# Performance work log

Measured on AMD Instinct MI355X. Metric: run time of the kernel, lower is better.

The kernel has to match this reference:

```python
import jax, jax.numpy as jnp
import numpy as np

E, D, H, O, K = 8, 1024, 4096, 1024, 2
N = 4096


def setup_inputs() -> dict:
    key = jax.random.key(0)
    ks = jax.random.split(key, 8)
    s_in = 1.0 / np.sqrt(D)
    s_h = 1.0 / np.sqrt(H)
    return {
        "x": jax.random.normal(ks[0], (N, D), dtype=jnp.float32),
        "W1": jax.random.uniform(ks[1], (E, D, H), jnp.float32, -s_in, s_in),
        "b1": jax.random.uniform(ks[2], (E, H), jnp.float32, -s_in, s_in),
        "W2": jax.random.uniform(ks[3], (E, H, O), jnp.float32, -s_h, s_h),
        "b2": jax.random.uniform(ks[4], (E, O), jnp.float32, -s_h, s_h),
        "Wg": jax.random.uniform(ks[5], (D, E), jnp.float32, -s_in, s_in),
        "bg": jax.random.uniform(ks[6], (E,), jnp.float32, -s_in, s_in),
    }


def reference(x, W1, b1, W2, b2, Wg, bg):
    # gate: [N, E] -> top-k logits and expert ids
    gate_logits = x @ Wg + bg
    topv, topi = jax.lax.top_k(gate_logits, K)          # [N, K]
    weights = jax.nn.softmax(topv, axis=-1)             # softmax over the k selected logits

    # dense all-expert MLP, then gather the selected experts per token
    h = jax.nn.relu(jnp.einsum("nd,edh->enh", x, W1) + b1[:, None, :])  # [E, N, H]
    y = jnp.einsum("enh,eho->eno", h, W2) + b2[:, None, :]              # [E, N, O]

    sel = y[topi, jnp.arange(N)[:, None]]               # [N, K, O]
    return jnp.sum(weights[..., None] * sel, axis=1)    # [N, O]
```

## Files before the change

kernel.cpp:

```cpp
#include <hip/hip_runtime.h>
#include <hip/hip_bf16.h>
#include <cstdint>

typedef __bf16 bf16;
typedef bf16 bf16x8 __attribute__((ext_vector_type(8)));
typedef bf16 bf16x4 __attribute__((ext_vector_type(4)));
typedef float f32x4 __attribute__((ext_vector_type(4)));

#define N_TOK 4096
#define DIM   1024
#define HID   4096
#define OUTD  1024
#define NEXP  8

__device__ __forceinline__ void async_copy16(const void* g, void* l) {
  __builtin_amdgcn_global_load_lds(
      (const __attribute__((address_space(1))) void*)g,
      (__attribute__((address_space(3))) void*)l, 16, 0, 0);
}

__device__ __forceinline__ void stage_tile2(
    const bf16* pA0, const bf16* pA1, const bf16* pA2, const bf16* pA3,
    const bf16* pB0, const bf16* pB1, const bf16* pB2, const bf16* pB3,
    bf16* lA, bf16* lB, int ko, int wave)
{
  async_copy16(pA0 + ko, lA + (wave * 4 + 0) * 512);
  async_copy16(pA1 + ko, lA + (wave * 4 + 1) * 512);
  async_copy16(pA2 + ko, lA + (wave * 4 + 2) * 512);
  async_copy16(pA3 + ko, lA + (wave * 4 + 3) * 512);
  async_copy16(pB0 + ko, lB + (wave * 4 + 0) * 512);
  async_copy16(pB1 + ko, lB + (wave * 4 + 1) * 512);
  async_copy16(pB2 + ko, lB + (wave * 4 + 2) * 512);
  async_copy16(pB3 + ko, lB + (wave * 4 + 3) * 512);
}

__global__ __launch_bounds__(256) void gate_kernel(
    const float* __restrict__ x, const float* __restrict__ Wg,
    const float* __restrict__ bg, int* __restrict__ topE, float* __restrict__ topW)
{
  int wave = threadIdx.x >> 6, lane = threadIdx.x & 63;
  int t = blockIdx.x * 4 + wave;
  float acc[8];
#pragma unroll
  for (int e = 0; e < 8; ++e) acc[e] = 0.f;
  const float* xrow = x + (size_t)t * DIM;
#pragma unroll
  for (int i = 0; i < DIM / 64; ++i) {
    int d = i * 64 + lane;
    float xv = xrow[d];
    float4 w0 = *(const float4*)(Wg + d * 8);
    float4 w1 = *(const float4*)(Wg + d * 8 + 4);
    acc[0] += xv * w0.x; acc[1] += xv * w0.y; acc[2] += xv * w0.z; acc[3] += xv * w0.w;
    acc[4] += xv * w1.x; acc[5] += xv * w1.y; acc[6] += xv * w1.z; acc[7] += xv * w1.w;
  }
#pragma unroll
  for (int off = 32; off > 0; off >>= 1) {
#pragma unroll
    for (int e = 0; e < 8; ++e) acc[e] += __shfl_xor(acc[e], off, 64);
  }
  if (lane == 0) {
    float l[8];
#pragma unroll
    for (int e = 0; e < 8; ++e) l[e] = acc[e] + bg[e];
    int e1 = 0;
#pragma unroll
    for (int e = 1; e < 8; ++e) if (l[e] > l[e1]) e1 = e;
    int e2 = (e1 == 0) ? 1 : 0;
#pragma unroll
    for (int e = 0; e < 8; ++e) if (e != e1 && l[e] > l[e2]) e2 = e;
    float w1 = 1.f / (1.f + __expf(l[e2] - l[e1]));
    topE[t * 2] = e1; topE[t * 2 + 1] = e2;
    topW[t * 2] = w1; topW[t * 2 + 1] = 1.f - w1;
  }
}

__global__ __launch_bounds__(256) void build_lists(
    const int* __restrict__ topE, const float* __restrict__ topW,
    int* __restrict__ cnt, int* __restrict__ tok_list, float* __restrict__ w_list,
    int* __restrict__ inv)
{
  __shared__ int lcnt[8], lbase[8];
  int tid = threadIdx.x;
  if (tid < 8) lcnt[tid] = 0;
  __syncthreads();
  int t = blockIdx.x * 256 + tid;
  int e1 = topE[2 * t], e2 = topE[2 * t + 1];
  float w1 = topW[2 * t], w2 = topW[2 * t + 1];
  int p1 = atomicAdd(&lcnt[e1], 1);
  int p2 = atomicAdd(&lcnt[e2], 1);
  __syncthreads();
  if (tid < 8) lbase[tid] = atomicAdd(&cnt[tid], lcnt[tid]);
  __syncthreads();
  int i1 = e1 * N_TOK + lbase[e1] + p1;
  int i2 = e2 * N_TOK + lbase[e2] + p2;
  tok_list[i1] = t; w_list[i1] = w1;
  tok_list[i2] = t; w_list[i2] = w2;
  inv[2 * t] = i1;
  inv[2 * t + 1] = i2;
}

__global__ void scan_kernel(const int* __restrict__ cnt, int* __restrict__ base)
{
  if (threadIdx.x == 0) {
    int s = 0;
    for (int e = 0; e < 8; ++e) { base[e] = s; s += cnt[e]; }
    base[8] = s;
  }
}

__global__ __launch_bounds__(256) void gather_cvt(
    const float* __restrict__ x, const int* __restrict__ tok_list,
    const int* __restrict__ base, bf16* __restrict__ xg)
{
  int wave = threadIdx.x >> 6, lane = threadIdx.x & 63;
  int s = blockIdx.x * 4 + wave;
  int e = 0;
#pragma unroll
  for (int i = 1; i < 8; ++i) e += (s >= base[i]);
  int tok = tok_list[e * N_TOK + (s - base[e])];
  const float4* src = (const float4*)(x + (size_t)tok * DIM);
  bf16x4* dst = (bf16x4*)(xg + (size_t)s * DIM);
#pragma unroll
  for (int i = 0; i < DIM / 256; ++i) {
    float4 v = src[i * 64 + lane];
    bf16x4 o;
    o.x = (bf16)v.x; o.y = (bf16)v.y; o.z = (bf16)v.z; o.w = (bf16)v.w;
    dst[i * 64 + lane] = o;
  }
}

__global__ __launch_bounds__(256) void transpose_cvt(
    const float* __restrict__ src, bf16* __restrict__ dst, int R, int C)
{
  __shared__ bf16 tile[64][68];
  int e = blockIdx.z;
  const float* s = src + (size_t)e * R * C;
  bf16* d = dst + (size_t)e * R * C;
  int c0 = blockIdx.x * 64, r0 = blockIdx.y * 64;
  int tid = threadIdx.x;
  int rr = tid >> 4;
  int cc = (tid & 15) * 4;
#pragma unroll
  for (int i = 0; i < 4; ++i) {
    int r = i * 16 + rr;
    float4 v = *(const float4*)(s + (size_t)(r0 + r) * C + c0 + cc);
    tile[cc + 0][r] = (bf16)v.x;
    tile[cc + 1][r] = (bf16)v.y;
    tile[cc + 2][r] = (bf16)v.z;
    tile[cc + 3][r] = (bf16)v.w;
  }
  __syncthreads();
#pragma unroll
  for (int i = 0; i < 4; ++i) {
    int ct = i * 16 + rr;
    bf16x4 o = *(const bf16x4*)&tile[ct][cc];
    *(bf16x4*)(d + (size_t)(c0 + ct) * R + r0 + cc) = o;
  }
}

__global__ __launch_bounds__(256) void gemm1_kernel(
    const bf16* __restrict__ xg, const bf16* __restrict__ W1t,
    const float* __restrict__ b1, bf16* __restrict__ hbuf,
    const int* __restrict__ cnt, const int* __restrict__ base)
{
  int e = blockIdx.z;
  int M = cnt[e];
  int mt = blockIdx.y;
  if (mt * 128 >= M) return;
  int nt = blockIdx.x;
  int b0 = base[e];

  __shared__ bf16 As[2 * 8192];
  __shared__ bf16 Bs[2 * 8192];

  int tid = threadIdx.x;
  int wave = tid >> 6, lane = tid & 63;
  int crow = lane >> 3;
  int ck   = ((lane & 7) ^ crow) * 8;

  const bf16* pA[4]; const bf16* pB[4];
#pragma unroll
  for (int i = 0; i < 4; ++i) {
    int ra = (wave * 4 + i) * 8 + crow;
    int lm = min(mt * 128 + ra, M - 1);
    pA[i] = xg + (size_t)(b0 + lm) * DIM + ck;
    pB[i] = W1t + ((size_t)e * HID + nt * 128 + ra) * DIM + ck;
  }

  int wm = wave & 1, wn = wave >> 1;
  int quad = lane >> 4, lr = lane & 15;
  int sw = lr & 7;
  f32x4 acc[4][4] = {};

  const int NKT = DIM / 64;
  stage_tile2(pA[0], pA[1], pA[2], pA[3], pB[0], pB[1], pB[2], pB[3], As, Bs, 0, wave);
  __syncthreads();

  for (int kt = 0; kt < NKT; ++kt) {
    int cur = kt & 1;
    if (kt + 1 < NKT)
      stage_tile2(pA[0], pA[1], pA[2], pA[3], pB[0], pB[1], pB[2], pB[3],
                  As + (cur ^ 1) * 8192, Bs + (cur ^ 1) * 8192, (kt + 1) * 64, wave);
    const bf16* Asb = As + cur * 8192;
    const bf16* Bsb = Bs + cur * 8192;
#pragma unroll
    for (int kk = 0; kk < 2; ++kk) {
      bf16x8 af[4], bfr[4];
#pragma unroll
      for (int i = 0; i < 4; ++i)
        af[i] = *(const bf16x8*)(Asb + (wm * 64 + i * 16 + lr) * 64 + (((kk * 4 + quad) ^ sw) * 8));
#pragma unroll
      for (int j = 0; j < 4; ++j)
        bfr[j] = *(const bf16x8*)(Bsb + (wn * 64 + j * 16 + lr) * 64 + (((kk * 4 + quad) ^ sw) * 8));
#pragma unroll
      for (int i = 0; i < 4; ++i)
#pragma unroll
        for (int j = 0; j < 4; ++j)
          acc[i][j] = __builtin_amdgcn_mfma_f32_16x16x32_bf16(af[i], bfr[j], acc[i][j], 0, 0, 0);
    }
    __syncthreads();
  }

#pragma unroll
  for (int j = 0; j < 4; ++j) {
    int col = nt * 128 + wn * 64 + j * 16 + lr;
    float bias = b1[e * HID + col];
#pragma unroll
    for (int i = 0; i < 4; ++i) {
#pragma unroll
      for (int r = 0; r < 4; ++r) {
        int lm = mt * 128 + wm * 64 + i * 16 + quad * 4 + r;
        if (lm < M) {
          float v = acc[i][j][r] + bias;
          hbuf[(size_t)(b0 + lm) * HID + col] = (bf16)fmaxf(v, 0.f);
        }
      }
    }
  }
}

__global__ __launch_bounds__(256) void gemm2_kernel(
    const bf16* __restrict__ hbuf, const bf16* __restrict__ W2t,
    const float* __restrict__ b2, float* __restrict__ ybufA, float* __restrict__ ybufB,
    const int* __restrict__ cnt, const int* __restrict__ base)
{
  int e = blockIdx.z;
  int M = cnt[e];
  int mt = blockIdx.y;
  if (mt * 128 >= M) return;
  int nt = blockIdx.x;
  int b0 = base[e];

  __shared__ bf16 As[2 * 8192];
  __shared__ bf16 Bs[2 * 8192];

  int tid = threadIdx.x;
  int wave = tid >> 6, lane = tid & 63;
  int crow = lane >> 3;
  int ck   = ((lane & 7) ^ crow) * 8;

  const bf16* pA[4]; const bf16* pB[4];
#pragma unroll
  for (int i = 0; i < 4; ++i) {
    int ra = (wave * 4 + i) * 8 + crow;
    int lm = min(mt * 128 + ra, M - 1);
    pA[i] = hbuf + (size_t)(b0 + lm) * HID + ck;
    pB[i] = W2t + ((size_t)e * OUTD + nt * 128 + ra) * HID + ck;
  }

  int wm = wave & 1, wn = wave >> 1;
  int quad = lane >> 4, lr = lane & 15;
  int sw = lr & 7;
  f32x4 acc[4][4] = {};

  const int NKT = HID / 64;
  stage_tile2(pA[0], pA[1], pA[2], pA[3], pB[0], pB[1], pB[2], pB[3], As, Bs, 0, wave);
  __syncthreads();

  for (int kt = 0; kt < NKT; ++kt) {
    int cur = kt & 1;
    if (kt + 1 < NKT)
      stage_tile2(pA[0], pA[1], pA[2], pA[3], pB[0], pB[1], pB[2], pB[3],
                  As + (cur ^ 1) * 8192, Bs + (cur ^ 1) * 8192, (kt + 1) * 64, wave);
    const bf16* Asb = As + cur * 8192;
    const bf16* Bsb = Bs + cur * 8192;
#pragma unroll
    for (int kk = 0; kk < 2; ++kk) {
      bf16x8 af[4], bfr[4];
#pragma unroll
      for (int i = 0; i < 4; ++i)
        af[i] = *(const bf16x8*)(Asb + (wm * 64 + i * 16 + lr) * 64 + (((kk * 4 + quad) ^ sw) * 8));
#pragma unroll
      for (int j = 0; j < 4; ++j)
        bfr[j] = *(const bf16x8*)(Bsb + (wn * 64 + j * 16 + lr) * 64 + (((kk * 4 + quad) ^ sw) * 8));
#pragma unroll
      for (int i = 0; i < 4; ++i)
#pragma unroll
        for (int j = 0; j < 4; ++j)
          acc[i][j] = __builtin_amdgcn_mfma_f32_16x16x32_bf16(af[i], bfr[j], acc[i][j], 0, 0, 0);
    }
    __syncthreads();
  }

#pragma unroll
  for (int j = 0; j < 4; ++j) {
    int col = nt * 128 + wn * 64 + j * 16 + lr;
    float bias = b2[e * OUTD + col];
#pragma unroll
    for (int i = 0; i < 4; ++i) {
#pragma unroll
      for (int r = 0; r < 4; ++r) {
        int lm = mt * 128 + wm * 64 + i * 16 + quad * 4 + r;
        if (lm < M) {
          int slot = b0 + lm;
          float* yr = (slot < 4096) ? (ybufA + (size_t)slot * OUTD)
                                    : (ybufB + (size_t)(slot - 4096) * OUTD);
          yr[col] = acc[i][j][r] + bias;
        }
      }
    }
  }
}

__global__ __launch_bounds__(256) void combine_kernel(
    const float* __restrict__ ybufA, const float* __restrict__ ybufB,
    const int* __restrict__ inv, const float* __restrict__ topW,
    const int* __restrict__ base, float* __restrict__ out)
{
  int wave = threadIdx.x >> 6, lane = threadIdx.x & 63;
  int t = blockIdx.x * 4 + wave;
  int i0 = inv[2 * t], i1 = inv[2 * t + 1];
  float w0 = topW[2 * t], w1 = topW[2 * t + 1];
  int s0 = base[i0 >> 12] + (i0 & (N_TOK - 1));
  int s1 = base[i1 >> 12] + (i1 & (N_TOK - 1));
  const float4* r0 = (const float4*)((s0 < 4096) ? (ybufA + (size_t)s0 * OUTD)
                                                 : (ybufB + (size_t)(s0 - 4096) * OUTD));
  const float4* r1 = (const float4*)((s1 < 4096) ? (ybufA + (size_t)s1 * OUTD)
                                                 : (ybufB + (size_t)(s1 - 4096) * OUTD));
  float4* o = (float4*)(out + (size_t)t * OUTD);
#pragma unroll
  for (int i = 0; i < OUTD / 256; ++i) {
    float4 a = r0[i * 64 + lane];
    float4 b = r1[i * 64 + lane];
    float4 c;
    c.x = w0 * a.x + w1 * b.x;
    c.y = w0 * a.y + w1 * b.y;
    c.z = w0 * a.z + w1 * b.z;
    c.w = w0 * a.w + w1 * b.w;
    o[i * 64 + lane] = c;
  }
}

extern "C" void kernel_launch(void* const* d_in, const int* in_sizes, int n_in,
                              void* d_out, int out_size, void* d_ws, size_t ws_size,
                              hipStream_t stream)
{
  (void)in_sizes; (void)n_in; (void)ws_size; (void)out_size;
  const float* x  = (const float*)d_in[0];
  const float* W1 = (const float*)d_in[1];
  const float* b1 = (const float*)d_in[2];
  const float* W2 = (const float*)d_in[3];
  const float* b2 = (const float*)d_in[4];
  const float* Wg = (const float*)d_in[5];
  const float* bg = (const float*)d_in[6];
  float* out = (float*)d_out;

  char* ws = (char*)d_ws;
  int*   tok_list = (int*)(ws + 0);
  float* w_list   = (float*)(ws + 131072);
  int*   topE     = (int*)(ws + 262144);
  float* topW     = (float*)(ws + 294912);
  int*   cnt      = (int*)(ws + 327680);
  int*   base     = (int*)(ws + 327744);
  int*   inv      = (int*)(ws + 327808);
  bf16*  xg    = (bf16*)(ws + 393216);
  bf16*  W1t   = (bf16*)(ws + 17170432);
  bf16*  hbuf  = (bf16*)(ws + 84279296);
  bf16*  W2t   = (bf16*)(ws + 393216);
  float* ybufA = (float*)(ws + 67502080);
  float* ybufB = (float*)(ws + 151388160);

  hipMemsetAsync(cnt, 0, 64, stream);

  gate_kernel<<<dim3(N_TOK / 4), 256, 0, stream>>>(x, Wg, bg, topE, topW);
  build_lists<<<dim3(N_TOK / 256), 256, 0, stream>>>(topE, topW, cnt, tok_list, w_list, inv);
  scan_kernel<<<dim3(1), 64, 0, stream>>>(cnt, base);
  gather_cvt<<<dim3(2 * N_TOK / 4), 256, 0, stream>>>(x, tok_list, base, xg);
  transpose_cvt<<<dim3(HID / 64, DIM / 64, NEXP), 256, 0, stream>>>(W1, W1t, DIM, HID);
  gemm1_kernel<<<dim3(HID / 128, N_TOK / 128, NEXP), 256, 0, stream>>>(xg, W1t, b1, hbuf, cnt, base);
  transpose_cvt<<<dim3(OUTD / 64, HID / 64, NEXP), 256, 0, stream>>>(W2, W2t, HID, OUTD);
  gemm2_kernel<<<dim3(OUTD / 128, N_TOK / 128, NEXP), 256, 0, stream>>>(hbuf, W2t, b2, ybufA, ybufB, cnt, base);
  combine_kernel<<<dim3(N_TOK / 4), 256, 0, stream>>>(ybufA, ybufB, inv, topW, base, out);
}
```

Baseline: 695.0 us.

## Prefetch two K-tiles ahead with explicit vmcnt waits in expert GEMMs

```diff
diff --git a/kernel.cpp b/kernel.cpp
--- a/kernel.cpp
+++ b/kernel.cpp
@@ -19,7 +19,7 @@
       (__attribute__((address_space(3))) void*)l, 16, 0, 0);
 }
 
-__device__ __forceinline__ void stage_tile2(
+__device__ __forceinline__ void stage_tile(
     const bf16* pA0, const bf16* pA1, const bf16* pA2, const bf16* pA3,
     const bf16* pB0, const bf16* pB1, const bf16* pB2, const bf16* pB3,
     bf16* lA, bf16* lB, int ko, int wave)
@@ -170,8 +170,8 @@
   int nt = blockIdx.x;
   int b0 = base[e];
 
-  __shared__ bf16 As[2 * 8192];
-  __shared__ bf16 Bs[2 * 8192];
+  __shared__ bf16 As[2][128 * 64];
+  __shared__ bf16 Bs[2][128 * 64];
 
   int tid = threadIdx.x;
   int wave = tid >> 6, lane = tid & 63;
@@ -193,16 +193,21 @@
   f32x4 acc[4][4] = {};
 
   const int NKT = DIM / 64;
-  stage_tile2(pA[0], pA[1], pA[2], pA[3], pB[0], pB[1], pB[2], pB[3], As, Bs, 0, wave);
-  __syncthreads();
+  stage_tile(pA[0], pA[1], pA[2], pA[3], pB[0], pB[1], pB[2], pB[3],
+             As[0], Bs[0], 0, wave);
+  stage_tile(pA[0], pA[1], pA[2], pA[3], pB[0], pB[1], pB[2], pB[3],
+             As[1], Bs[1], 64, wave);
 
   for (int kt = 0; kt < NKT; ++kt) {
     int cur = kt & 1;
-    if (kt + 1 < NKT)
-      stage_tile2(pA[0], pA[1], pA[2], pA[3], pB[0], pB[1], pB[2], pB[3],
-                  As + (cur ^ 1) * 8192, Bs + (cur ^ 1) * 8192, (kt + 1) * 64, wave);
-    const bf16* Asb = As + cur * 8192;
-    const bf16* Bsb = Bs + cur * 8192;
+    if (kt < NKT - 1) asm volatile("s_waitcnt vmcnt(8)" ::: "memory");
+    else              asm volatile("s_waitcnt vmcnt(0)" ::: "memory");
+    __builtin_amdgcn_sched_barrier(0);
+    __builtin_amdgcn_s_barrier();
+    __builtin_amdgcn_sched_barrier(0);
+
+    const bf16* Asb = As[cur];
+    const bf16* Bsb = Bs[cur];
 #pragma unroll
     for (int kk = 0; kk < 2; ++kk) {
       bf16x8 af[4], bfr[4];
@@ -218,7 +223,14 @@
         for (int j = 0; j < 4; ++j)
           acc[i][j] = __builtin_amdgcn_mfma_f32_16x16x32_bf16(af[i], bfr[j], acc[i][j], 0, 0, 0);
     }
-    __syncthreads();
+
+    asm volatile("s_waitcnt lgkmcnt(0)" ::: "memory");
+    __builtin_amdgcn_sched_barrier(0);
+    __builtin_amdgcn_s_barrier();
+    __builtin_amdgcn_sched_barrier(0);
+    if (kt + 2 < NKT)
+      stage_tile(pA[0], pA[1], pA[2], pA[3], pB[0], pB[1], pB[2], pB[3],
+                 As[cur], Bs[cur], (kt + 2) * 64, wave);
   }
 
 #pragma unroll
@@ -251,8 +263,8 @@
   int nt = blockIdx.x;
   int b0 = base[e];
 
-  __shared__ bf16 As[2 * 8192];
-  __shared__ bf16 Bs[2 * 8192];
+  __shared__ bf16 As[2][128 * 64];
+  __shared__ bf16 Bs[2][128 * 64];
 
   int tid = threadIdx.x;
   int wave = tid >> 6, lane = tid & 63;
@@ -274,16 +286,21 @@
   f32x4 acc[4][4] = {};
 
   const int NKT = HID / 64;
-  stage_tile2(pA[0], pA[1], pA[2], pA[3], pB[0], pB[1], pB[2], pB[3], As, Bs, 0, wave);
-  __syncthreads();
+  stage_tile(pA[0], pA[1], pA[2], pA[3], pB[0], pB[1], pB[2], pB[3],
+             As[0], Bs[0], 0, wave);
+  stage_tile(pA[0], pA[1], pA[2], pA[3], pB[0], pB[1], pB[2], pB[3],
+             As[1], Bs[1], 64, wave);
 
   for (int kt = 0; kt < NKT; ++kt) {
     int cur = kt & 1;
-    if (kt + 1 < NKT)
-      stage_tile2(pA[0], pA[1], pA[2], pA[3], pB[0], pB[1], pB[2], pB[3],
-                  As + (cur ^ 1) * 8192, Bs + (cur ^ 1) * 8192, (kt + 1) * 64, wave);
-    const bf16* Asb = As + cur * 8192;
-    const bf16* Bsb = Bs + cur * 8192;
+    if (kt < NKT - 1) asm volatile("s_waitcnt vmcnt(8)" ::: "memory");
+    else              asm volatile("s_waitcnt vmcnt(0)" ::: "memory");
+    __builtin_amdgcn_sched_barrier(0);
+    __builtin_amdgcn_s_barrier();
+    __builtin_amdgcn_sched_barrier(0);
+
+    const bf16* Asb = As[cur];
+    const bf16* Bsb = Bs[cur];
 #pragma unroll
     for (int kk = 0; kk < 2; ++kk) {
       bf16x8 af[4], bfr[4];
@@ -299,7 +316,14 @@
         for (int j = 0; j < 4; ++j)
           acc[i][j] = __builtin_amdgcn_mfma_f32_16x16x32_bf16(af[i], bfr[j], acc[i][j], 0, 0, 0);
     }
-    __syncthreads();
+
+    asm volatile("s_waitcnt lgkmcnt(0)" ::: "memory");
+    __builtin_amdgcn_sched_barrier(0);
+    __builtin_amdgcn_s_barrier();
+    __builtin_amdgcn_sched_barrier(0);
+    if (kt + 2 < NKT)
+      stage_tile(pA[0], pA[1], pA[2], pA[3], pB[0], pB[1], pB[2], pB[3],
+                 As[cur], Bs[cur], (kt + 2) * 64, wave);
   }
 
 #pragma unroll
```

New measurement: 642.7 us. 7.5% less time.
